# Kernel tuning notes

Measured on AMD Instinct MI355X. Metric: run time of the kernel, lower is better.

Reference implementation:

```python
import jax, jax.numpy as jnp
import numpy as np

B, T, D, K = 8, 4096, 1024, 4096

def setup_inputs() -> dict:
    key = jax.random.key(0)
    kx, kc = jax.random.split(key)
    x = jax.random.normal(kx, (B, T, D), dtype=jnp.float32)
    C = jax.random.normal(kc, (D, K), dtype=jnp.float32)  # centroids stored as [d, K]
    Cnorm = jnp.sum(C * C, axis=0, keepdims=True)  # [1, K], matches torch precompute
    return {"x": x, "C": C, "Cnorm": Cnorm}

def reference(x, C, Cnorm):
    batched = x.ndim == 3
    if batched:
        b, t, d = x.shape
        x2 = x.reshape(-1, d)  # [N, d]
    else:
        x2 = x
    dist = jnp.sum(x2 * x2, axis=1, keepdims=True) - 2.0 * (x2 @ C) + Cnorm
    assigned = jnp.argmin(dist, axis=1)
    if batched:
        assigned = assigned.reshape(b, t)
    return assigned
```

## Files before the change

kernel.cpp:

```cpp
#include <hip/hip_runtime.h>
#include <cstdint>
#include <cstddef>

typedef _Float16 half8 __attribute__((ext_vector_type(8)));
typedef _Float16 half4 __attribute__((ext_vector_type(4)));
typedef float    floatx4 __attribute__((ext_vector_type(4)));

constexpr int N_ROWS = 32768;
constexpr int D_DIM  = 1024;
constexpr int K_CENT = 4096;
constexpr int CAP    = 4096;
constexpr int KSL    = 2;
constexpr int RSL    = 8;
constexpr float EPS_GAP = 0.4f;

__device__ __forceinline__ void gload_lds16(const void* g, void* l) {
    __builtin_amdgcn_global_load_lds(
        (const __attribute__((address_space(1))) uint32_t*)g,
        (__attribute__((address_space(3))) uint32_t*)l, 16, 0, 0);
}

__global__ __launch_bounds__(256) void convert_C_kernel(
    const float* __restrict__ C, _Float16* __restrict__ ChiT, _Float16* __restrict__ CloT)
{
    __shared__ float tile[32][33];
    const int bk = blockIdx.x, bd = blockIdx.y, t = threadIdx.x;
    const int r = t >> 3, c4 = (t & 7) * 4;
    const float4 v = *(const float4*)&C[(size_t)(bd * 32 + r) * K_CENT + bk * 32 + c4];
    tile[r][c4 + 0] = v.x; tile[r][c4 + 1] = v.y;
    tile[r][c4 + 2] = v.z; tile[r][c4 + 3] = v.w;
    __syncthreads();
    half4 h, l;
#pragma unroll
    for (int i = 0; i < 4; ++i) {
        const float f = tile[c4 + i][r];
        const _Float16 hi = (_Float16)f;
        h[i] = hi;
        l[i] = (_Float16)(f - (float)hi);
    }
    *(half4*)&ChiT[(size_t)(bk * 32 + r) * D_DIM + bd * 32 + c4] = h;
    *(half4*)&CloT[(size_t)(bk * 32 + r) * D_DIM + bd * 32 + c4] = l;
}

__global__ __launch_bounds__(256) void convert_x_kernel(
    const float* __restrict__ x, _Float16* __restrict__ xh)
{
    const size_t g = (size_t)blockIdx.x * 256 + threadIdx.x;
    const float4 v0 = *(const float4*)&x[g * 8];
    const float4 v1 = *(const float4*)&x[g * 8 + 4];
    half8 h;
    h[0] = (_Float16)v0.x; h[1] = (_Float16)v0.y; h[2] = (_Float16)v0.z; h[3] = (_Float16)v0.w;
    h[4] = (_Float16)v1.x; h[5] = (_Float16)v1.y; h[6] = (_Float16)v1.z; h[7] = (_Float16)v1.w;
    *(half8*)&xh[g * 8] = h;
}

constexpr int P_XH = 0;
constexpr int P_CH = 4096;
constexpr int P_HB = 12288;

__device__ __forceinline__ void stage6(
    _Float16* buf, const _Float16* __restrict__ xh, const _Float16* __restrict__ ChiT,
    int row0, int kc, int kd, int wid, int scol, int skg)
{
#pragma unroll
    for (int q = 0; q < 2; ++q) {
        const int sub = wid * 2 + q;
        gload_lds16(&xh[(size_t)(row0 + sub * 16 + scol) * D_DIM + kd + skg * 8],
                    buf + P_XH + sub * 512);
    }
#pragma unroll
    for (int q = 0; q < 4; ++q) {
        const int sub = wid * 4 + q;
        gload_lds16(&ChiT[(size_t)(kc + sub * 16 + scol) * D_DIM + kd + skg * 8],
                    buf + P_CH + sub * 512);
    }
}

__global__ __launch_bounds__(256, 2) void kmeans_pass1(
    const _Float16* __restrict__ xh, const _Float16* __restrict__ ChiT,
    const float* __restrict__ Cnorm,
    float* __restrict__ m1buf, int* __restrict__ i1buf, float* __restrict__ m2buf)
{
    __shared__ _Float16 lds[2][P_HB];
    __shared__ float red_d[2][64][2];
    __shared__ int   red_i[2][64][2];
    __shared__ float red_2[2][64][2];
    __shared__ float cns[K_CENT / KSL];

    const int bid  = blockIdx.x;
    const int xcd  = bid & 7;
    const int ks   = xcd & 1;
    const int rb   = (bid >> 3) * 4 + (xcd >> 1);
    const int row0 = rb * 128;
    const int kb0  = ks * (K_CENT / KSL);

    const int tid  = threadIdx.x;
    const int lane = tid & 63;
    const int wid  = tid >> 6;
    const int wm   = wid >> 1;
    const int wn   = wid & 1;

    const int l15 = lane & 15;
    const int l4  = lane >> 4;
    const int kge = l4 ^ ((l15 >> 1) & 3);
    const int fragoff = l15 * 32 + kge * 8;

    const int scol = lane >> 2;
    const int skg  = (lane & 3) ^ ((scol >> 1) & 3);

#pragma unroll
    for (int q = 0; q < (K_CENT / KSL) / 256; ++q)
        cns[q * 256 + tid] = Cnorm[kb0 + q * 256 + tid];

    float rm1 = 3.4e38f, rm2 = 3.4e38f;
    int   ri1 = 0;

    stage6(lds[0], xh, ChiT, row0, kb0, 0, wid, scol, skg);

    const int nch = (K_CENT / KSL) / 256;
    for (int ci = 0; ci < nch; ++ci) {
        const int kc = kb0 + ci * 256;
        floatx4 acc[4][8];
#pragma unroll
        for (int i = 0; i < 4; ++i)
#pragma unroll
            for (int j = 0; j < 8; ++j) acc[i][j] = (floatx4)0.0f;

        for (int kdi = 0; kdi < 32; ++kdi) {
            _Float16* bufc = lds[kdi & 1];
            _Float16* bufn = lds[(kdi + 1) & 1];
            const bool hn = (kdi < 31) || (ci < nch - 1);
            if (hn) {
                const int nkc = (kdi < 31) ? kc : kc + 256;
                const int nkd = (kdi < 31) ? (kdi + 1) * 32 : 0;
                stage6(bufn, xh, ChiT, row0, nkc, nkd, wid, scol, skg);
                asm volatile("s_waitcnt vmcnt(6)" ::: "memory");
            } else {
                asm volatile("s_waitcnt vmcnt(0)" ::: "memory");
            }
            __builtin_amdgcn_s_barrier();
            __builtin_amdgcn_sched_barrier(0);

            half8 ah[4], bh[8];
#pragma unroll
            for (int i = 0; i < 4; ++i)
                ah[i] = *(const half8*)(bufc + P_XH + (wm * 4 + i) * 512 + fragoff);
#pragma unroll
            for (int j = 0; j < 8; ++j)
                bh[j] = *(const half8*)(bufc + P_CH + (wn * 8 + j) * 512 + fragoff);

            __builtin_amdgcn_s_setprio(1);
#pragma unroll
            for (int i = 0; i < 4; ++i)
#pragma unroll
                for (int j = 0; j < 8; ++j)
                    acc[i][j] = __builtin_amdgcn_mfma_f32_16x16x32_f16(ah[i], bh[j], acc[i][j], 0, 0, 0);
            __builtin_amdgcn_s_setprio(0);

            __builtin_amdgcn_sched_barrier(0);
            asm volatile("" ::: "memory");
            __builtin_amdgcn_s_barrier();
        }

        const int colw = ci * 256 + wn * 128;
#pragma unroll
        for (int i = 0; i < 4; ++i)
#pragma unroll
            for (int r = 0; r < 4; ++r) {
                float m1 = 3.4e38f, m2 = 3.4e38f;
                int   i1 = 0;
#pragma unroll
                for (int j = 0; j < 8; ++j) {
                    const float cn = cns[colw + j * 16 + l15];
                    const float d  = fmaf(-2.0f, acc[i][j][r], cn);
                    const int   ix = kb0 + colw + j * 16 + l15;
                    if (d < m1) { m2 = m1; m1 = d; i1 = ix; }
                    else if (d < m2) { m2 = d; }
                }
#pragma unroll
                for (int off = 1; off < 16; off <<= 1) {
                    const float om1 = __shfl_xor(m1, off, 64);
                    const int   oi  = __shfl_xor(i1, off, 64);
                    const float om2 = __shfl_xor(m2, off, 64);
                    const float nm2 = fminf(fminf(m2, om2), fmaxf(m1, om1));
                    if (om1 < m1 || (om1 == m1 && oi < i1)) { m1 = om1; i1 = oi; }
                    m2 = nm2;
                }
                if (l15 == 0) {
                    const int rr = i * 16 + l4 * 4 + r;
                    red_d[wm][rr][wn] = m1;
                    red_i[wm][rr][wn] = i1;
                    red_2[wm][rr][wn] = m2;
                }
            }
        asm volatile("s_waitcnt lgkmcnt(0)" ::: "memory");
        __builtin_amdgcn_s_barrier();
        __builtin_amdgcn_sched_barrier(0);

        if (tid < 128) {
            const int hh = tid >> 6;
            const int rr = tid & 63;
            float m1 = red_d[hh][rr][0], m2 = red_2[hh][rr][0];
            int   i1 = red_i[hh][rr][0];
            const float om1 = red_d[hh][rr][1];
            const int   oi  = red_i[hh][rr][1];
            const float om2 = red_2[hh][rr][1];
            m2 = fminf(fminf(m2, om2), fmaxf(m1, om1));
            if (om1 < m1 || (om1 == m1 && oi < i1)) { m1 = om1; i1 = oi; }
            const float nm2 = fminf(fminf(rm2, m2), fmaxf(rm1, m1));
            if (m1 < rm1 || (m1 == rm1 && i1 < ri1)) { rm1 = m1; ri1 = i1; }
            rm2 = nm2;
        }
    }

    if (tid < 128) {
        const size_t off = (size_t)ks * N_ROWS + row0 + tid;
        m1buf[off] = rm1;
        i1buf[off] = ri1;
        m2buf[off] = rm2;
    }
}

__global__ __launch_bounds__(256) void kmeans_merge4(
    const float* __restrict__ m1buf, const int* __restrict__ i1buf,
    const float* __restrict__ m2buf, int* __restrict__ out,
    int* __restrict__ urows, unsigned int* __restrict__ ucount)
{
    const int row = blockIdx.x * 256 + threadIdx.x;
    float m1 = m1buf[row], m2 = m2buf[row];
    int   i1 = i1buf[row];
#pragma unroll
    for (int s = 1; s < KSL; ++s) {
        const float om1 = m1buf[(size_t)s * N_ROWS + row];
        const float om2 = m2buf[(size_t)s * N_ROWS + row];
        const int   oi  = i1buf[(size_t)s * N_ROWS + row];
        const float nm2 = fminf(fminf(m2, om2), fmaxf(m1, om1));
        if (om1 < m1 || (om1 == m1 && oi < i1)) { m1 = om1; i1 = oi; }
        m2 = nm2;
    }
    out[row] = i1;
    if (m2 - m1 <= EPS_GAP) {
        const unsigned slot = atomicAdd(ucount, 1u);
        if (slot < (unsigned)CAP) urows[slot] = row;
    }
}

__global__ __launch_bounds__(64) void kmeans_gather(
    const float* __restrict__ x, const int* __restrict__ urows,
    const unsigned int* __restrict__ ucount,
    _Float16* __restrict__ xch, _Float16* __restrict__ xcl)
{
    const unsigned cntr = *ucount;
    const unsigned cnt = cntr > (unsigned)CAP ? (unsigned)CAP : cntr;
    const unsigned slot = blockIdx.x;
    if (slot >= cnt) return;
    const int row = urows[slot];
    const int t = threadIdx.x;
#pragma unroll
    for (int e = 0; e < 16; ++e) {
        const int idx = e * 64 + t;
        const float v = x[(size_t)row * D_DIM + idx];
        const _Float16 h = (_Float16)v;
        xch[(size_t)slot * D_DIM + idx] = h;
        xcl[(size_t)slot * D_DIM + idx] = (_Float16)(v - (float)h);
    }
}

constexpr int R_XH = 0;
constexpr int R_XL = 1024;
constexpr int R_CH = 2048;
constexpr int R_CL = 10240;
constexpr int R_HB = 18432;

__global__ __launch_bounds__(256) void kmeans_rescore2(
    const _Float16* __restrict__ xch, const _Float16* __restrict__ xcl,
    const _Float16* __restrict__ ChiT, const _Float16* __restrict__ CloT,
    const float* __restrict__ Cnorm, const unsigned int* __restrict__ ucount,
    float* __restrict__ rpd, int* __restrict__ rpi)
{
    const unsigned cntr = *ucount;
    const unsigned cnt = cntr > (unsigned)CAP ? (unsigned)CAP : cntr;
    const int bid = blockIdx.x;
    const int ksl = bid & 7;
    const int grp = bid >> 3;
    if ((unsigned)(grp * 32) >= cnt) return;

    __shared__ _Float16 lds[2][R_HB];
    __shared__ float rd[32][4];
    __shared__ int   ri[32][4];

    const int tid  = threadIdx.x;
    const int lane = tid & 63;
    const int wid  = tid >> 6;
    const int l15  = lane & 15;
    const int l4   = lane >> 4;
    const int kge  = l4 ^ ((l15 >> 1) & 3);
    const int fragoff = l15 * 32 + kge * 8;
    const int scol = lane >> 2;
    const int skg  = (lane & 3) ^ ((scol >> 1) & 3);

    const int base  = grp * 32;
    const int kbase = ksl * (K_CENT / RSL);

    float best[2][4];
    int   bidx[2][4];
#pragma unroll
    for (int i = 0; i < 2; ++i)
#pragma unroll
        for (int r = 0; r < 4; ++r) { best[i][r] = 3.4e38f; bidx[i][r] = 0; }

    for (int ch = 0; ch < 2; ++ch) {
        const int kc = kbase + ch * 256;
        floatx4 acc[2][4];
#pragma unroll
        for (int i = 0; i < 2; ++i)
#pragma unroll
            for (int j = 0; j < 4; ++j) acc[i][j] = (floatx4)0.0f;

        {
            _Float16* buf = lds[0];
#pragma unroll
            for (int q = 0; q < 4; ++q) {
                const int sub = wid * 4 + q;
                gload_lds16(&ChiT[(size_t)(kc + sub * 16 + scol) * D_DIM + 0 + skg * 8], buf + R_CH + sub * 512);
                gload_lds16(&CloT[(size_t)(kc + sub * 16 + scol) * D_DIM + 0 + skg * 8], buf + R_CL + sub * 512);
            }
            if (wid < 2)
                gload_lds16(&xch[(size_t)(base + wid * 16 + scol) * D_DIM + 0 + skg * 8], buf + R_XH + wid * 512);
            else
                gload_lds16(&xcl[(size_t)(base + (wid - 2) * 16 + scol) * D_DIM + 0 + skg * 8], buf + R_XL + (wid - 2) * 512);
            __syncthreads();
        }

        for (int kdi = 0; kdi < D_DIM / 32; ++kdi) {
            const int cur = kdi & 1;
            _Float16* bufc = lds[cur];
            _Float16* bufn = lds[cur ^ 1];
            const int  kdn = (kdi + 1) * 32;
            const bool pf  = (kdi + 1 < D_DIM / 32);

            if (pf) {
#pragma unroll
                for (int q = 0; q < 4; ++q) {
                    const int sub = wid * 4 + q;
                    gload_lds16(&ChiT[(size_t)(kc + sub * 16 + scol) * D_DIM + kdn + skg * 8], bufn + R_CH + sub * 512);
                    gload_lds16(&CloT[(size_t)(kc + sub * 16 + scol) * D_DIM + kdn + skg * 8], bufn + R_CL + sub * 512);
                }
                if (wid < 2)
                    gload_lds16(&xch[(size_t)(base + wid * 16 + scol) * D_DIM + kdn + skg * 8], bufn + R_XH + wid * 512);
                else
                    gload_lds16(&xcl[(size_t)(base + (wid - 2) * 16 + scol) * D_DIM + kdn + skg * 8], bufn + R_XL + (wid - 2) * 512);
            }

            half8 ah[2], al[2], bh[4], bl[4];
#pragma unroll
            for (int i = 0; i < 2; ++i) {
                ah[i] = *(const half8*)(bufc + R_XH + i * 512 + fragoff);
                al[i] = *(const half8*)(bufc + R_XL + i * 512 + fragoff);
            }
#pragma unroll
            for (int j = 0; j < 4; ++j) {
                bh[j] = *(const half8*)(bufc + R_CH + (wid * 4 + j) * 512 + fragoff);
                bl[j] = *(const half8*)(bufc + R_CL + (wid * 4 + j) * 512 + fragoff);
            }
#pragma unroll
            for (int i = 0; i < 2; ++i)
#pragma unroll
                for (int j = 0; j < 4; ++j) {
                    acc[i][j] = __builtin_amdgcn_mfma_f32_16x16x32_f16(ah[i], bh[j], acc[i][j], 0, 0, 0);
                    acc[i][j] = __builtin_amdgcn_mfma_f32_16x16x32_f16(ah[i], bl[j], acc[i][j], 0, 0, 0);
                    acc[i][j] = __builtin_amdgcn_mfma_f32_16x16x32_f16(al[i], bh[j], acc[i][j], 0, 0, 0);
                }
            __syncthreads();
        }

#pragma unroll
        for (int j = 0; j < 4; ++j) {
            const int col = kc + wid * 64 + j * 16 + l15;
            const float cn = Cnorm[col];
#pragma unroll
            for (int i = 0; i < 2; ++i)
#pragma unroll
                for (int r = 0; r < 4; ++r) {
                    const float d = fmaf(-2.0f, acc[i][j][r], cn);
                    if (d < best[i][r]) { best[i][r] = d; bidx[i][r] = col; }
                }
        }
    }

#pragma unroll
    for (int i = 0; i < 2; ++i)
#pragma unroll
        for (int r = 0; r < 4; ++r) {
            float m1 = best[i][r];
            int   i1 = bidx[i][r];
#pragma unroll
            for (int off = 1; off < 16; off <<= 1) {
                const float om1 = __shfl_xor(m1, off, 64);
                const int   oi  = __shfl_xor(i1, off, 64);
                if (om1 < m1 || (om1 == m1 && oi < i1)) { m1 = om1; i1 = oi; }
            }
            if (l15 == 0) { rd[i * 16 + l4 * 4 + r][wid] = m1; ri[i * 16 + l4 * 4 + r][wid] = i1; }
        }
    __syncthreads();

    if (tid < 32) {
        float m1 = rd[tid][0];
        int   i1 = ri[tid][0];
#pragma unroll
        for (int w = 1; w < 4; ++w) {
            const float om1 = rd[tid][w];
            const int   oi  = ri[tid][w];
            if (om1 < m1 || (om1 == m1 && oi < i1)) { m1 = om1; i1 = oi; }
        }
        rpd[(size_t)(base + tid) * RSL + ksl] = m1;
        rpi[(size_t)(base + tid) * RSL + ksl] = i1;
    }
}

__global__ __launch_bounds__(256) void kmeans_merge2(
    const float* __restrict__ rpd, const int* __restrict__ rpi,
    const int* __restrict__ urows, const unsigned int* __restrict__ ucount,
    int* __restrict__ out)
{
    const unsigned cntr = *ucount;
    const unsigned cnt = cntr > (unsigned)CAP ? (unsigned)CAP : cntr;
    const unsigned s = blockIdx.x * 256 + threadIdx.x;
    if (s >= cnt) return;
    float m1 = rpd[(size_t)s * RSL];
    int   i1 = rpi[(size_t)s * RSL];
#pragma unroll
    for (int k = 1; k < RSL; ++k) {
        const float om = rpd[(size_t)s * RSL + k];
        const int   oi = rpi[(size_t)s * RSL + k];
        if (om < m1 || (om == m1 && oi < i1)) { m1 = om; i1 = oi; }
    }
    out[urows[s]] = i1;
}

constexpr int F_XH = 0, F_XL = 4096, F_CH = 8192, F_CL = 16384, F_HB = 24576;

__device__ __forceinline__ void write_x2(_Float16* buf, const float4 v, int r, int kb) {
    const _Float16 h0 = (_Float16)v.x, h1 = (_Float16)v.y;
    const _Float16 h2 = (_Float16)v.z, h3 = (_Float16)v.w;
    const int kg  = kb >> 3;
    const int hs  = (kb >> 2) & 1;
    const int kge = kg ^ ((r >> 1) & 3);
    const int base = (r >> 4) * 512 + (r & 15) * 32 + kge * 8 + hs * 4;
    *(half4*)(buf + F_XH + base) = (half4){h0, h1, h2, h3};
    *(half4*)(buf + F_XL + base) = (half4){(_Float16)(v.x - (float)h0), (_Float16)(v.y - (float)h1),
                                           (_Float16)(v.z - (float)h2), (_Float16)(v.w - (float)h3)};
}

__global__ __launch_bounds__(512, 2) void kmeans_mfma_kernel(
    const float* __restrict__ x, const _Float16* __restrict__ ChiT,
    const _Float16* __restrict__ CloT, const float* __restrict__ Cnorm,
    int* __restrict__ out)
{
    __shared__ _Float16 lds[2][F_HB];
    __shared__ float red_d[2][64][4];
    __shared__ int   red_i[2][64][4];

    const int tid  = threadIdx.x;
    const int lane = tid & 63;
    const int wid  = tid >> 6;
    const int wm   = wid >> 2;
    const int wn   = wid & 3;
    const int row0 = blockIdx.x * 128;
    const int l15 = lane & 15;
    const int l4  = lane >> 4;
    const int kge = l4 ^ ((l15 >> 1) & 3);
    const int fragoff = l15 * 32 + kge * 8;
    const int sr = tid >> 2, sc = tid & 3;
    const int ccol = lane >> 2;
    const int ckg  = (lane & 3) ^ ((ccol >> 1) & 3);

    float best[4][4];
    int   bidx[4][4];
#pragma unroll
    for (int i = 0; i < 4; ++i)
#pragma unroll
        for (int r = 0; r < 4; ++r) { best[i][r] = 3.4e38f; bidx[i][r] = 0; }

    for (int kc = 0; kc < K_CENT; kc += 256) {
        floatx4 acc[4][4];
#pragma unroll
        for (int i = 0; i < 4; ++i)
#pragma unroll
            for (int j = 0; j < 4; ++j) acc[i][j] = (floatx4)0.0f;
        {
            _Float16* buf = lds[0];
            const float4 xv0 = *(const float4*)&x[(size_t)(row0 + sr) * D_DIM + 0 + sc * 4];
            const float4 xv1 = *(const float4*)&x[(size_t)(row0 + sr) * D_DIM + 16 + sc * 4];
            gload_lds16(&ChiT[(size_t)(kc + wid * 16 + ccol) * D_DIM + 0 + ckg * 8], buf + F_CH + wid * 512);
            gload_lds16(&ChiT[(size_t)(kc + (wid + 8) * 16 + ccol) * D_DIM + 0 + ckg * 8], buf + F_CH + (wid + 8) * 512);
            gload_lds16(&CloT[(size_t)(kc + wid * 16 + ccol) * D_DIM + 0 + ckg * 8], buf + F_CL + wid * 512);
            gload_lds16(&CloT[(size_t)(kc + (wid + 8) * 16 + ccol) * D_DIM + 0 + ckg * 8], buf + F_CL + (wid + 8) * 512);
            write_x2(buf, xv0, sr, sc * 4);
            write_x2(buf, xv1, sr, sc * 4 + 16);
            __syncthreads();
        }
        for (int kdi = 0; kdi < D_DIM / 32; ++kdi) {
            const int cur = kdi & 1;
            _Float16* bufc = lds[cur];
            _Float16* bufn = lds[cur ^ 1];
            const int  kdn = (kdi + 1) * 32;
            const bool pf  = (kdi + 1 < D_DIM / 32);
            float4 xv0, xv1;
            if (pf) {
                xv0 = *(const float4*)&x[(size_t)(row0 + sr) * D_DIM + kdn + sc * 4];
                xv1 = *(const float4*)&x[(size_t)(row0 + sr) * D_DIM + kdn + 16 + sc * 4];
                gload_lds16(&ChiT[(size_t)(kc + wid * 16 + ccol) * D_DIM + kdn + ckg * 8], bufn + F_CH + wid * 512);
                gload_lds16(&ChiT[(size_t)(kc + (wid + 8) * 16 + ccol) * D_DIM + kdn + ckg * 8], bufn + F_CH + (wid + 8) * 512);
                gload_lds16(&CloT[(size_t)(kc + wid * 16 + ccol) * D_DIM + kdn + ckg * 8], bufn + F_CL + wid * 512);
                gload_lds16(&CloT[(size_t)(kc + (wid + 8) * 16 + ccol) * D_DIM + kdn + ckg * 8], bufn + F_CL + (wid + 8) * 512);
            }
            half8 ah[4], al[4], bh[4], bl[4];
#pragma unroll
            for (int i = 0; i < 4; ++i) {
                ah[i] = *(const half8*)(bufc + F_XH + (wm * 4 + i) * 512 + fragoff);
                al[i] = *(const half8*)(bufc + F_XL + (wm * 4 + i) * 512 + fragoff);
            }
#pragma unroll
            for (int j = 0; j < 4; ++j) {
                bh[j] = *(const half8*)(bufc + F_CH + (wn * 4 + j) * 512 + fragoff);
                bl[j] = *(const half8*)(bufc + F_CL + (wn * 4 + j) * 512 + fragoff);
            }
#pragma unroll
            for (int i = 0; i < 4; ++i)
#pragma unroll
                for (int j = 0; j < 4; ++j) {
                    acc[i][j] = __builtin_amdgcn_mfma_f32_16x16x32_f16(ah[i], bh[j], acc[i][j], 0, 0, 0);
                    acc[i][j] = __builtin_amdgcn_mfma_f32_16x16x32_f16(ah[i], bl[j], acc[i][j], 0, 0, 0);
                    acc[i][j] = __builtin_amdgcn_mfma_f32_16x16x32_f16(al[i], bh[j], acc[i][j], 0, 0, 0);
                }
            if (pf) {
                write_x2(bufn, xv0, sr, sc * 4);
                write_x2(bufn, xv1, sr, sc * 4 + 16);
            }
            __syncthreads();
        }
        const int colw = kc + wn * 64;
#pragma unroll
        for (int ns = 0; ns < 4; ++ns) {
            const float cn = Cnorm[colw + ns * 16 + l15];
            const int   ix = colw + ns * 16 + l15;
#pragma unroll
            for (int i = 0; i < 4; ++i)
#pragma unroll
                for (int r = 0; r < 4; ++r) {
                    const float d = fmaf(-2.0f, acc[i][ns][r], cn);
                    if (d < best[i][r]) { best[i][r] = d; bidx[i][r] = ix; }
                }
        }
    }
#pragma unroll
    for (int i = 0; i < 4; ++i)
#pragma unroll
        for (int r = 0; r < 4; ++r) {
            float d  = best[i][r];
            int   ix = bidx[i][r];
#pragma unroll
            for (int off = 1; off < 16; off <<= 1) {
                const float od = __shfl_xor(d, off, 64);
                const int   oi = __shfl_xor(ix, off, 64);
                if (od < d || (od == d && oi < ix)) { d = od; ix = oi; }
            }
            if (l15 == 0) {
                red_d[wm][i * 16 + l4 * 4 + r][wn] = d;
                red_i[wm][i * 16 + l4 * 4 + r][wn] = ix;
            }
        }
    __syncthreads();
    if (tid < 128) {
        const int hh = tid >> 6, rr = tid & 63;
        float bd = red_d[hh][rr][0];
        int   bi2 = red_i[hh][rr][0];
#pragma unroll
        for (int w = 1; w < 4; ++w) {
            const float od = red_d[hh][rr][w];
            const int   oi = red_i[hh][rr][w];
            if (od < bd || (od == bd && oi < bi2)) { bd = od; bi2 = oi; }
        }
        out[row0 + tid] = bi2;
    }
}

__global__ __launch_bounds__(256, 2) void kmeans_assign_f32(
    const float* __restrict__ x, const float* __restrict__ Cm,
    const float* __restrict__ Cnorm, int* __restrict__ out)
{
    __shared__ float xs[32][64];
    __shared__ float cs[32][64];
    const int tid = threadIdx.x;
    const int tx = tid & 15, ty = tid >> 4;
    const int row0 = blockIdx.x * 64;
    const int xr = tid >> 3, xc = tid & 7;
    const int cr = tid >> 4, cc = tid & 15;
    float best[4]; int bidx[4];
#pragma unroll
    for (int i = 0; i < 4; ++i) { best[i] = 3.4e38f; bidx[i] = 0; }
    for (int kc = 0; kc < K_CENT; kc += 64) {
        float acc[16];
#pragma unroll
        for (int i = 0; i < 16; ++i) acc[i] = 0.0f;
        for (int kd = 0; kd < D_DIM; kd += 32) {
            const float4 xv0 = *(const float4*)&x[(size_t)(row0 + xr) * D_DIM + kd + xc * 4];
            const float4 xv1 = *(const float4*)&x[(size_t)(row0 + xr + 32) * D_DIM + kd + xc * 4];
            const float4 cv0 = *(const float4*)&Cm[(size_t)(kd + cr) * K_CENT + kc + cc * 4];
            const float4 cv1 = *(const float4*)&Cm[(size_t)(kd + cr + 16) * K_CENT + kc + cc * 4];
            __syncthreads();
            xs[xc*4+0][xr] = xv0.x; xs[xc*4+1][xr] = xv0.y; xs[xc*4+2][xr] = xv0.z; xs[xc*4+3][xr] = xv0.w;
            xs[xc*4+0][xr+32] = xv1.x; xs[xc*4+1][xr+32] = xv1.y; xs[xc*4+2][xr+32] = xv1.z; xs[xc*4+3][xr+32] = xv1.w;
            *(float4*)&cs[cr][cc*4]    = cv0;
            *(float4*)&cs[cr+16][cc*4] = cv1;
            __syncthreads();
#pragma unroll
            for (int kk = 0; kk < 32; ++kk) {
                const float4 a = *(const float4*)&xs[kk][ty*4];
                const float4 b = *(const float4*)&cs[kk][tx*4];
                acc[ 0] += a.x*b.x; acc[ 1] += a.x*b.y; acc[ 2] += a.x*b.z; acc[ 3] += a.x*b.w;
                acc[ 4] += a.y*b.x; acc[ 5] += a.y*b.y; acc[ 6] += a.y*b.z; acc[ 7] += a.y*b.w;
                acc[ 8] += a.z*b.x; acc[ 9] += a.z*b.y; acc[10] += a.z*b.z; acc[11] += a.z*b.w;
                acc[12] += a.w*b.x; acc[13] += a.w*b.y; acc[14] += a.w*b.z; acc[15] += a.w*b.w;
            }
        }
        const float4 cn = *(const float4*)&Cnorm[kc + tx*4];
        const float cnv[4] = {cn.x, cn.y, cn.z, cn.w};
#pragma unroll
        for (int i = 0; i < 4; ++i)
#pragma unroll
            for (int j = 0; j < 4; ++j) {
                const float dist = cnv[j] - 2.0f * acc[i*4+j];
                const int   idx  = kc + tx*4 + j;
                if (dist < best[i]) { best[i] = dist; bidx[i] = idx; }
            }
    }
#pragma unroll
    for (int i = 0; i < 4; ++i) {
        float d = best[i]; int ix = bidx[i];
#pragma unroll
        for (int off = 1; off < 16; off <<= 1) {
            const float od = __shfl_xor(d, off, 64);
            const int   oi = __shfl_xor(ix, off, 64);
            if (od < d || (od == d && oi < ix)) { d = od; ix = oi; }
        }
        if (tx == 0) out[row0 + ty*4 + i] = ix;
    }
}

extern "C" void kernel_launch(void* const* d_in, const int* in_sizes, int n_in,
                              void* d_out, int out_size, void* d_ws, size_t ws_size,
                              hipStream_t stream) {
    const float* x     = (const float*)d_in[0];
    const float* C     = (const float*)d_in[1];
    const float* Cnorm = (const float*)d_in[2];
    int* out = (int*)d_out;

    const size_t chalf = (size_t)K_CENT * D_DIM;
    const size_t capd  = (size_t)CAP * D_DIM;
    const size_t xhN   = (size_t)N_ROWS * D_DIM;

    const size_t sz_base = (2 * chalf + 2 * capd) * 2
                         + (size_t)KSL * N_ROWS * 12
                         + (size_t)CAP * RSL * 8
                         + (size_t)CAP * 4 + 64;
    const size_t need_full = sz_base + xhN * 2;
    const size_t need_r3   = 2 * chalf * 2;

    if (ws_size >= need_full) {
        _Float16* ChiT = (_Float16*)d_ws;
        _Float16* CloT = ChiT + chalf;
        _Float16* xch  = CloT + chalf;
        _Float16* xcl  = xch + capd;
        float* m1buf = (float*)(xcl + capd);
        float* m2buf = m1buf + (size_t)KSL * N_ROWS;
        int*   i1buf = (int*)(m2buf + (size_t)KSL * N_ROWS);
        float* rpd   = (float*)(i1buf + (size_t)KSL * N_ROWS);
        int*   rpi   = (int*)(rpd + (size_t)CAP * RSL);
        int*   urows = rpi + (size_t)CAP * RSL;
        unsigned int* ucount = (unsigned int*)(urows + CAP);
        _Float16* xh = (_Float16*)(ucount + 16);

        convert_C_kernel<<<dim3(128, 32), 256, 0, stream>>>(C, ChiT, CloT);
        convert_x_kernel<<<dim3((int)(xhN / 2048)), 256, 0, stream>>>(x, xh);
        hipMemsetAsync(ucount, 0, sizeof(unsigned int), stream);
        kmeans_pass1<<<dim3(256 * KSL), 256, 0, stream>>>(xh, ChiT, Cnorm, m1buf, i1buf, m2buf);
        kmeans_merge4<<<dim3(N_ROWS / 256), 256, 0, stream>>>(m1buf, i1buf, m2buf, out, urows, ucount);
        kmeans_gather<<<dim3(CAP), 64, 0, stream>>>(x, urows, ucount, xch, xcl);
        kmeans_rescore2<<<dim3((CAP / 32) * RSL), 256, 0, stream>>>(xch, xcl, ChiT, CloT, Cnorm, ucount, rpd, rpi);
        kmeans_merge2<<<dim3(CAP / 256), 256, 0, stream>>>(rpd, rpi, urows, ucount, out);
    } else if (ws_size >= need_r3) {
        _Float16* ChiT = (_Float16*)d_ws;
        _Float16* CloT = ChiT + chalf;
        convert_C_kernel<<<dim3(128, 32), 256, 0, stream>>>(C, ChiT, CloT);
        kmeans_mfma_kernel<<<dim3(N_ROWS / 128), 512, 0, stream>>>(x, ChiT, CloT, Cnorm, out);
    } else {
        kmeans_assign_f32<<<dim3(N_ROWS / 64), 256, 0, stream>>>(x, C, Cnorm, out);
    }
}
```

Baseline: 480.4 us.

## Triple-buffer LDS staging and flatten chunk loop into one pipelined step loop

Moves the pass-1 GEMM from double to triple LDS buffering with a prefetch distance of two, and flattens the centroid-chunk and depth loops into one step loop. The pipeline keeps running across chunk boundaries, and the epilogue argmin reduction runs inline every 32 steps. The Cnorm shared-memory cache is dropped; Cnorm is now read from global memory in the epilogue. The third buffer raises LDS use, which may limit occupancy at 2 blocks per CU, and the epilogue's global reads could stall.

```diff
diff --git a/kernel.cpp b/kernel.cpp
--- a/kernel.cpp
+++ b/kernel.cpp
@@ -81,11 +81,10 @@
     const float* __restrict__ Cnorm,
     float* __restrict__ m1buf, int* __restrict__ i1buf, float* __restrict__ m2buf)
 {
-    __shared__ _Float16 lds[2][P_HB];
+    __shared__ _Float16 lds[3][P_HB];
     __shared__ float red_d[2][64][2];
     __shared__ int   red_i[2][64][2];
     __shared__ float red_2[2][64][2];
-    __shared__ float cns[K_CENT / KSL];
 
     const int bid  = blockIdx.x;
     const int xcd  = bid & 7;
@@ -108,108 +107,122 @@
     const int scol = lane >> 2;
     const int skg  = (lane & 3) ^ ((scol >> 1) & 3);
 
-#pragma unroll
-    for (int q = 0; q < (K_CENT / KSL) / 256; ++q)
-        cns[q * 256 + tid] = Cnorm[kb0 + q * 256 + tid];
-
     float rm1 = 3.4e38f, rm2 = 3.4e38f;
     int   ri1 = 0;
 
-    stage6(lds[0], xh, ChiT, row0, kb0, 0, wid, scol, skg);
-
-    const int nch = (K_CENT / KSL) / 256;
-    for (int ci = 0; ci < nch; ++ci) {
-        const int kc = kb0 + ci * 256;
-        floatx4 acc[4][8];
+    constexpr int NSTEP = ((K_CENT / KSL) / 256) * 32;
+
+    stage6(lds[0], xh, ChiT, row0, kb0, 0,  wid, scol, skg);
+    stage6(lds[1], xh, ChiT, row0, kb0, 32, wid, scol, skg);
+
+    floatx4 acc[4][8];
+#pragma unroll
+    for (int i = 0; i < 4; ++i)
+#pragma unroll
+        for (int j = 0; j < 8; ++j) acc[i][j] = (floatx4)0.0f;
+
+    int cur = 0;
+    for (int s = 0; s < NSTEP; ++s) {
+        _Float16* bufc = lds[cur];
+        const int s2 = s + 2;
+        if (s2 < NSTEP) {
+            const int nkc = kb0 + (s2 >> 5) * 256;
+            const int nkd = (s2 & 31) * 32;
+            const int b2  = (cur >= 1) ? cur - 1 : 2;
+            stage6(lds[b2], xh, ChiT, row0, nkc, nkd, wid, scol, skg);
+            asm volatile("s_waitcnt vmcnt(12)" ::: "memory");
+        } else if (s + 1 < NSTEP) {
+            asm volatile("s_waitcnt vmcnt(6)" ::: "memory");
+        } else {
+            asm volatile("s_waitcnt vmcnt(0)" ::: "memory");
+        }
+        __builtin_amdgcn_s_barrier();
+        __builtin_amdgcn_sched_barrier(0);
+
+        half8 ah[4], bh[8];
 #pragma unroll
         for (int i = 0; i < 4; ++i)
-#pragma unroll
-            for (int j = 0; j < 8; ++j) acc[i][j] = (floatx4)0.0f;
-
-        for (int kdi = 0; kdi < 32; ++kdi) {
-            _Float16* bufc = lds[kdi & 1];
-            _Float16* bufn = lds[(kdi + 1) & 1];
-            const bool hn = (kdi < 31) || (ci < nch - 1);
-            if (hn) {
-                const int nkc = (kdi < 31) ? kc : kc + 256;
-                const int nkd = (kdi < 31) ? (kdi + 1) * 32 : 0;
-                stage6(bufn, xh, ChiT, row0, nkc, nkd, wid, scol, skg);
-                asm volatile("s_waitcnt vmcnt(6)" ::: "memory");
-            } else {
-                asm volatile("s_waitcnt vmcnt(0)" ::: "memory");
-            }
+            ah[i] = *(const half8*)(bufc + P_XH + (wm * 4 + i) * 512 + fragoff);
+#pragma unroll
+        for (int j = 0; j < 8; ++j)
+            bh[j] = *(const half8*)(bufc + P_CH + (wn * 8 + j) * 512 + fragoff);
+
+        __builtin_amdgcn_s_setprio(1);
+#pragma unroll
+        for (int i = 0; i < 4; ++i)
+#pragma unroll
+            for (int j = 0; j < 8; ++j)
+                acc[i][j] = __builtin_amdgcn_mfma_f32_16x16x32_f16(ah[i], bh[j], acc[i][j], 0, 0, 0);
+        __builtin_amdgcn_s_setprio(0);
+
+        __builtin_amdgcn_sched_barrier(0);
+        asm volatile("" ::: "memory");
+        __builtin_amdgcn_s_barrier();
+
+        cur = (cur == 2) ? 0 : cur + 1;
+
+        if ((s & 31) == 31) {
+            const int ci   = s >> 5;
+            const int colw = ci * 256 + wn * 128;
+            float cn8[8];
+#pragma unroll
+            for (int j = 0; j < 8; ++j) cn8[j] = Cnorm[kb0 + colw + j * 16 + l15];
+
+#pragma unroll
+            for (int i = 0; i < 4; ++i)
+#pragma unroll
+                for (int r = 0; r < 4; ++r) {
+                    float m1 = 3.4e38f, m2 = 3.4e38f;
+                    int   i1 = 0;
+#pragma unroll
+                    for (int j = 0; j < 8; ++j) {
+                        const float d  = fmaf(-2.0f, acc[i][j][r], cn8[j]);
+                        const int   ix = kb0 + colw + j * 16 + l15;
+                        if (d < m1) { m2 = m1; m1 = d; i1 = ix; }
+                        else if (d < m2) { m2 = d; }
+                    }
+#pragma unroll
+                    for (int off = 1; off < 16; off <<= 1) {
+                        const float om1 = __shfl_xor(m1, off, 64);
+                        const int   oi  = __shfl_xor(i1, off, 64);
+                        const float om2 = __shfl_xor(m2, off, 64);
+                        const float nm2 = fminf(fminf(m2, om2), fmaxf(m1, om1));
+                        if (om1 < m1 || (om1 == m1 && oi < i1)) { m1 = om1; i1 = oi; }
+                        m2 = nm2;
+                    }
+                    if (l15 == 0) {
+                        const int rr = i * 16 + l4 * 4 + r;
+                        red_d[wm][rr][wn] = m1;
+                        red_i[wm][rr][wn] = i1;
+                        red_2[wm][rr][wn] = m2;
+                    }
+                }
+            asm volatile("s_waitcnt lgkmcnt(0)" ::: "memory");
             __builtin_amdgcn_s_barrier();
             __builtin_amdgcn_sched_barrier(0);
 
-            half8 ah[4], bh[8];
+            if (tid < 128) {
+                const int hh = tid >> 7;
+                const int rr = tid & 127;
+                const int h2 = rr >> 6;
+                const int r2 = rr & 63;
+                float m1 = red_d[h2][r2][0], m2 = red_2[h2][r2][0];
+                int   i1 = red_i[h2][r2][0];
+                const float om1 = red_d[h2][r2][1];
+                const int   oi  = red_i[h2][r2][1];
+                const float om2 = red_2[h2][r2][1];
+                m2 = fminf(fminf(m2, om2), fmaxf(m1, om1));
+                if (om1 < m1 || (om1 == m1 && oi < i1)) { m1 = om1; i1 = oi; }
+                const float nm2 = fminf(fminf(rm2, m2), fmaxf(rm1, m1));
+                if (m1 < rm1 || (m1 == rm1 && i1 < ri1)) { rm1 = m1; ri1 = i1; }
+                rm2 = nm2;
+                (void)hh;
+            }
+
 #pragma unroll
             for (int i = 0; i < 4; ++i)
-                ah[i] = *(const half8*)(bufc + P_XH + (wm * 4 + i) * 512 + fragoff);
-#pragma unroll
-            for (int j = 0; j < 8; ++j)
-                bh[j] = *(const half8*)(bufc + P_CH + (wn * 8 + j) * 512 + fragoff);
-
-            __builtin_amdgcn_s_setprio(1);
-#pragma unroll
-            for (int i = 0; i < 4; ++i)
-#pragma unroll
-                for (int j = 0; j < 8; ++j)
-                    acc[i][j] = __builtin_amdgcn_mfma_f32_16x16x32_f16(ah[i], bh[j], acc[i][j], 0, 0, 0);
-            __builtin_amdgcn_s_setprio(0);
-
-            __builtin_amdgcn_sched_barrier(0);
-            asm volatile("" ::: "memory");
-            __builtin_amdgcn_s_barrier();
-        }
-
-        const int colw = ci * 256 + wn * 128;
-#pragma unroll
-        for (int i = 0; i < 4; ++i)
-#pragma unroll
-            for (int r = 0; r < 4; ++r) {
-                float m1 = 3.4e38f, m2 = 3.4e38f;
-                int   i1 = 0;
-#pragma unroll
-                for (int j = 0; j < 8; ++j) {
-                    const float cn = cns[colw + j * 16 + l15];
-                    const float d  = fmaf(-2.0f, acc[i][j][r], cn);
-                    const int   ix = kb0 + colw + j * 16 + l15;
-                    if (d < m1) { m2 = m1; m1 = d; i1 = ix; }
-                    else if (d < m2) { m2 = d; }
-                }
-#pragma unroll
-                for (int off = 1; off < 16; off <<= 1) {
-                    const float om1 = __shfl_xor(m1, off, 64);
-                    const int   oi  = __shfl_xor(i1, off, 64);
-                    const float om2 = __shfl_xor(m2, off, 64);
-                    const float nm2 = fminf(fminf(m2, om2), fmaxf(m1, om1));
-                    if (om1 < m1 || (om1 == m1 && oi < i1)) { m1 = om1; i1 = oi; }
-                    m2 = nm2;
-                }
-                if (l15 == 0) {
-                    const int rr = i * 16 + l4 * 4 + r;
-                    red_d[wm][rr][wn] = m1;
-                    red_i[wm][rr][wn] = i1;
-                    red_2[wm][rr][wn] = m2;
-                }
-            }
-        asm volatile("s_waitcnt lgkmcnt(0)" ::: "memory");
-        __builtin_amdgcn_s_barrier();
-        __builtin_amdgcn_sched_barrier(0);
-
-        if (tid < 128) {
-            const int hh = tid >> 6;
-            const int rr = tid & 63;
-            float m1 = red_d[hh][rr][0], m2 = red_2[hh][rr][0];
-            int   i1 = red_i[hh][rr][0];
-            const float om1 = red_d[hh][rr][1];
-            const int   oi  = red_i[hh][rr][1];
-            const float om2 = red_2[hh][rr][1];
-            m2 = fminf(fminf(m2, om2), fmaxf(m1, om1));
-            if (om1 < m1 || (om1 == m1 && oi < i1)) { m1 = om1; i1 = oi; }
-            const float nm2 = fminf(fminf(rm2, m2), fmaxf(rm1, m1));
-            if (m1 < rm1 || (m1 == rm1 && i1 < ri1)) { rm1 = m1; ri1 = i1; }
-            rm2 = nm2;
+#pragma unroll
+                for (int j = 0; j < 8; ++j) acc[i][j] = (floatx4)0.0f;
         }
     }
 
```

Result: no change. 476.2 us (-0.9%).
